# Performance work log

Measured on AMD Instinct MI355X. Metric: run time of the kernel, lower is better.

## Reference

```python
import jax, jax.numpy as jnp
import numpy as np

N = 50000          # nodes
E = 800000         # edges (avg degree 16)
NS = 0.01          # LeakyReLU negative slope
N_CONVS = 3


def setup_inputs() -> dict:
    key = jax.random.key(0)
    ks = jax.random.split(key, 12)
    g = lambda k, s: (jax.random.normal(k, s, dtype=jnp.float32) * 0.05)
    return dict(
        x=jax.random.normal(ks[0], (N, 16), dtype=jnp.float32),
        edge_index=jax.random.randint(ks[1], (2, E), 0, N),
        edge_weight=jax.random.uniform(ks[2], (E, 1), dtype=jnp.float32),
        # prep MLP: Linear(16,64)+LeakyReLU, Linear(64,64)+Tanh
        Wp_in=g(ks[3], (16, 64)), bp_in=jnp.zeros((64,), jnp.float32),
        Wp_h=g(ks[4], (64, 64)), bp_h=jnp.zeros((64,), jnp.float32),
        # per-conv edge projection Linear(edge_dim=1, 64), stacked over 3 convs
        We=g(ks[5], (N_CONVS, 1, 64)), be=jnp.zeros((N_CONVS, 64), jnp.float32),
        # per-conv nn MLP: Linear(64,64)+LeakyReLU, Linear(64,64)+Tanh
        Wm0=g(ks[6], (N_CONVS, 64, 64)), bm0=jnp.zeros((N_CONVS, 64), jnp.float32),
        Wm1=g(ks[7], (N_CONVS, 64, 64)), bm1=jnp.zeros((N_CONVS, 64), jnp.float32),
        # post MLP: Linear(64,64)+LeakyReLU, Linear(64,32)+Tanh
        Wq0=g(ks[8], (64, 64)), bq0=jnp.zeros((64,), jnp.float32),
        Wq1=g(ks[9], (64, 32)), bq1=jnp.zeros((32,), jnp.float32),
    )


def reference(x, edge_index, edge_weight,
              Wp_in, bp_in, Wp_h, bp_h,
              We, be, Wm0, bm0, Wm1, bm1,
              Wq0, bq0, Wq1, bq1):
    lrelu = lambda v: jax.nn.leaky_relu(v, NS)
    # prep MLP (dropout=0 -> no-op)
    h = lrelu(x @ Wp_in + bp_in)
    h = jnp.tanh(h @ Wp_h + bp_h)
    src, dst = edge_index[0], edge_index[1]
    # stacked GINEConv layers (eps=0): out = nn(x + sum_j ReLU(x_j + lin_e(e_ij)))
    for k in range(N_CONVS):
        e = edge_weight @ We[k] + be[k]              # [E,64] edge embedding
        msg = jax.nn.relu(h[src] + e)                # [E,64] gather + fuse
        agg = jax.ops.segment_sum(msg, dst, num_segments=N)  # [N,64] scatter-sum
        z = agg + h                                  # (1+eps)*x with eps=0
        z = lrelu(z @ Wm0[k] + bm0[k])
        h = jnp.tanh(z @ Wm1[k] + bm1[k])
    # post MLP
    z = lrelu(h @ Wq0 + bq0)
    return jnp.tanh(z @ Wq1 + bq1)                   # [N,32]
```

## Files before the change

kernel.cpp:

```cpp
#include <hip/hip_runtime.h>
#include <hip/hip_fp16.h>
#include <math.h>

#define NS 0.01f
#define CAP 48
#define QS (1.f / 65535.f)
#define POISON 0xAAAAAAAAu
#define ZS 72

typedef _Float16 f16;
typedef __attribute__((ext_vector_type(8))) f16 f16x8;
typedef __attribute__((ext_vector_type(4))) float f32x4;

__device__ __forceinline__ float lrelu(float v) { return fmaxf(v, NS * v); }

__device__ __forceinline__ unsigned rel_cnt(unsigned raw) {
    return min(raw, raw - POISON);
}

__global__ void __launch_bounds__(512) build_kernel(
    const int* __restrict__ src, const int* __restrict__ dst,
    const float* __restrict__ ew, int* __restrict__ cnt,
    unsigned* __restrict__ bucket, int E, int fillBlocks,
    const float* __restrict__ x,
    const float* __restrict__ Wp_in, const float* __restrict__ bp_in,
    const float* __restrict__ Wp_h,  const float* __restrict__ bp_h,
    __half* __restrict__ h, int N, int prepBlocks,
    const float* __restrict__ Wm0, const float* __restrict__ Wm1,
    const float* __restrict__ Wq0, const float* __restrict__ Wq1,
    __half* __restrict__ WTh)
{
    __shared__ float zt[64 * 65];
    const int b = (int)blockIdx.x;
    const int t = threadIdx.x;

    if (b < fillBlocks) {
        const int e0 = (b * 512 + t) * 8;
        if (e0 + 7 < E && (E & 7) == 0) {
            const int4   dA = *(const int4*)(dst + e0);
            const int4   dB = *(const int4*)(dst + e0 + 4);
            const int4   sA = *(const int4*)(src + e0);
            const int4   sB = *(const int4*)(src + e0 + 4);
            const float4 wA = *(const float4*)(ew + e0);
            const float4 wB = *(const float4*)(ew + e0 + 4);
            const int   dd[8] = {dA.x, dA.y, dA.z, dA.w, dB.x, dB.y, dB.z, dB.w};
            const int   ss[8] = {sA.x, sA.y, sA.z, sA.w, sB.x, sB.y, sB.z, sB.w};
            const float ww[8] = {wA.x, wA.y, wA.z, wA.w, wB.x, wB.y, wB.z, wB.w};
            unsigned p[8];
            #pragma unroll
            for (int q = 0; q < 8; ++q)
                p[q] = rel_cnt((unsigned)atomicAdd(&cnt[dd[q]], 1));
            #pragma unroll
            for (int q = 0; q < 8; ++q) {
                if (p[q] < CAP) {
                    const unsigned qq = __float2uint_rn(ww[q] * 65535.f) & 0xffffu;
                    __builtin_nontemporal_store(((unsigned)ss[q] << 16) | qq,
                                                &bucket[(size_t)dd[q] * CAP + p[q]]);
                }
            }
        } else {
            for (int e = e0; e < min(e0 + 8, E); ++e) {
                const int d = dst[e];
                const unsigned p = rel_cnt((unsigned)atomicAdd(&cnt[d], 1));
                if (p < CAP) {
                    const unsigned q = __float2uint_rn(ew[e] * 65535.f) & 0xffffu;
                    bucket[(size_t)d * CAP + p] = ((unsigned)src[e] << 16) | q;
                }
            }
        }
        return;
    }
    if (b < fillBlocks + prepBlocks) {
        const int n0 = (b - fillBlocks) * 64;
        #pragma unroll
        for (int r = 0; r < 2; ++r) {
            const int idx = r * 512 + t;
            const int nl = idx >> 4, i = idx & 15;
            const int n = n0 + nl;
            zt[nl * 65 + i] = (n < N) ? x[(size_t)n * 16 + i] : 0.f;
        }
        __syncthreads();
        const int lane = t & 63;
        const int w = __builtin_amdgcn_readfirstlane(t >> 6);
        float zx[16];
        #pragma unroll
        for (int i = 0; i < 16; ++i) zx[i] = zt[lane * 65 + i];
        float y[8];
        #pragma unroll
        for (int jj = 0; jj < 8; ++jj) {
            const int j = w * 8 + jj;
            float a = bp_in[j];
            #pragma unroll
            for (int i = 0; i < 16; ++i) a = fmaf(zx[i], Wp_in[i * 64 + j], a);
            y[jj] = lrelu(a);
        }
        __syncthreads();
        #pragma unroll
        for (int jj = 0; jj < 8; ++jj) zt[lane * 65 + w * 8 + jj] = y[jj];
        __syncthreads();
        #pragma unroll
        for (int jj = 0; jj < 8; ++jj) y[jj] = bp_h[w * 8 + jj];
        #pragma unroll
        for (int half = 0; half < 2; ++half) {
            float zh[32];
            #pragma unroll
            for (int i = 0; i < 32; ++i) zh[i] = zt[lane * 65 + half * 32 + i];
            #pragma unroll
            for (int jj = 0; jj < 8; ++jj) {
                const int j = w * 8 + jj;
                #pragma unroll
                for (int i = 0; i < 32; ++i)
                    y[jj] = fmaf(zh[i], Wp_h[(half * 32 + i) * 64 + j], y[jj]);
            }
        }
        __syncthreads();
        #pragma unroll
        for (int jj = 0; jj < 8; ++jj) zt[lane * 65 + w * 8 + jj] = tanhf(y[jj]);
        __syncthreads();
        #pragma unroll
        for (int r = 0; r < 8; ++r) {
            const int idx = r * 512 + t;
            const int nl = idx >> 6, i = idx & 63;
            const int n = n0 + nl;
            if (n < N) h[(size_t)n * 64 + i] = __float2half(zt[nl * 65 + i]);
        }
        return;
    }
    const int o = (b - fillBlocks - prepBlocks) * 512 + t;
    if (o >= 30720) return;
    float v;
    int d = o;
    if (d < 12288) {
        const int k = d >> 12, r = d & 4095, j = r >> 6, i = r & 63;
        v = Wm0[k * 4096 + i * 64 + j];
    } else if ((d -= 12288) < 12288) {
        const int k = d >> 12, r = d & 4095, j = r >> 6, i = r & 63;
        v = Wm1[k * 4096 + i * 64 + j];
    } else if ((d -= 12288) < 4096) {
        const int j = d >> 6, i = d & 63;
        v = Wq0[i * 64 + j];
    } else {
        d -= 4096;
        const int j = d >> 6, i = d & 63;
        v = Wq1[i * 32 + j];
    }
    WTh[o] = __float2half(v);
}

template<int ACT , int WLO >
__device__ __forceinline__ void mfma_layer64(
    const f16* __restrict__ inH, const f16* __restrict__ inL,
    const __half* __restrict__ WTh, const float* __restrict__ bias,
    int lane, int w, f16* __restrict__ outH, f16* __restrict__ outL)
{
    const int m   = w >> 1;
    const int nb0 = (w & 1) * 2;
    const int ar  = lane & 15;
    const int kg  = lane >> 4;
    const f16* ia = inH + (16 * m + ar) * ZS + kg * 8;
    const f16* il = inL + (16 * m + ar) * ZS + kg * 8;
    const f16x8 aH0 = *(const f16x8*)(ia);
    const f16x8 aH1 = *(const f16x8*)(ia + 32);
    const f16x8 aL0 = *(const f16x8*)(il);
    const f16x8 aL1 = *(const f16x8*)(il + 32);
    #pragma unroll
    for (int tt = 0; tt < 2; ++tt) {
        const int nb = nb0 + tt;
        const f16* wb = (const f16*)WTh + (16 * nb + ar) * 64 + kg * 8;
        const f16x8 b0 = *(const f16x8*)(wb);
        const f16x8 b1 = *(const f16x8*)(wb + 32);
        f32x4 c = {0.f, 0.f, 0.f, 0.f};
        c = __builtin_amdgcn_mfma_f32_16x16x32_f16(aH0, b0, c, 0, 0, 0);
        c = __builtin_amdgcn_mfma_f32_16x16x32_f16(aH1, b1, c, 0, 0, 0);
        c = __builtin_amdgcn_mfma_f32_16x16x32_f16(aL0, b0, c, 0, 0, 0);
        c = __builtin_amdgcn_mfma_f32_16x16x32_f16(aL1, b1, c, 0, 0, 0);
        const float bj = bias[16 * nb + ar];
        #pragma unroll
        for (int r = 0; r < 4; ++r) {
            float y = c[r] + bj;
            y = ACT ? lrelu(y) : tanhf(y);
            const int row = 16 * m + kg * 4 + r;
            const f16 hi = (f16)y;
            outH[row * ZS + 16 * nb + ar] = hi;
            if (WLO) outL[row * ZS + 16 * nb + ar] = (f16)(y - (float)hi);
        }
    }
}

__global__ void __launch_bounds__(512, 8) fused_conv_kernel(
    const __half* __restrict__ hin,
    const int* __restrict__ cnt,
    const unsigned* __restrict__ bucket,
    const float* __restrict__ We_k, const float* __restrict__ be_k,
    const __half* __restrict__ W0Th, const float* __restrict__ b0,
    const __half* __restrict__ W1Th, const float* __restrict__ b1,
    const __half* __restrict__ Wq0Th, const float* __restrict__ bq0,
    const __half* __restrict__ Wq1Th, const float* __restrict__ bq1,
    int do_post, __half* __restrict__ hout, float* __restrict__ out, int N)
{
    __shared__ __align__(16) f16 bAH[64 * ZS];
    __shared__ __align__(16) f16 bAL[64 * ZS];
    __shared__ __align__(16) f16 bBH[64 * ZS];
    __shared__ __align__(16) f16 bBL[64 * ZS];
    const int t = threadIdx.x;
    const int lane = t & 63;
    const int w = __builtin_amdgcn_readfirstlane(t >> 6);
    const int n0 = (int)blockIdx.x * 64;
    const float wej = We_k[lane], bej = be_k[lane];
    const float wqs = wej * QS;

    float acc[8];
    int   len[8];
    const int nb_ = n0 + w * 8;
    #pragma unroll
    for (int s = 0; s < 8; ++s) {
        const int n = nb_ + s;
        if (n < N) {
            acc[s] = __half2float(hin[(size_t)n * 64 + lane]);
            len[s] = __builtin_amdgcn_readfirstlane(
                         (int)min(rel_cnt((unsigned)cnt[n]), (unsigned)CAP));
        } else { acc[s] = 0.f; len[s] = 0; }
    }
    const unsigned* rows = bucket + (size_t)nb_ * CAP;

    int m[4];
    int maxLen = 0;
    #pragma unroll
    for (int pr = 0; pr < 4; ++pr) {
        m[pr] = max(len[2 * pr], len[2 * pr + 1]);
        maxLen = max(maxLen, m[pr]);
    }
    for (int p = 0; p < maxLen; p += 8) {
        #pragma unroll
        for (int pr = 0; pr < 4; ++pr) {
            if (p < m[pr]) {
                const uint4* rA = (const uint4*)(rows + (2 * pr) * CAP);
                const uint4* rB = (const uint4*)(rows + (2 * pr + 1) * CAP);
                const uint4 a0 = rA[p >> 2], a1 = rA[(p >> 2) + 1];
                const uint4 b0_ = rB[p >> 2], b1_ = rB[(p >> 2) + 1];
                unsigned rs[16];
                rs[0] = __builtin_amdgcn_readfirstlane(a0.x);
                rs[1] = __builtin_amdgcn_readfirstlane(a0.y);
                rs[2] = __builtin_amdgcn_readfirstlane(a0.z);
                rs[3] = __builtin_amdgcn_readfirstlane(a0.w);
                rs[4] = __builtin_amdgcn_readfirstlane(a1.x);
                rs[5] = __builtin_amdgcn_readfirstlane(a1.y);
                rs[6] = __builtin_amdgcn_readfirstlane(a1.z);
                rs[7] = __builtin_amdgcn_readfirstlane(a1.w);
                rs[8]  = __builtin_amdgcn_readfirstlane(b0_.x);
                rs[9]  = __builtin_amdgcn_readfirstlane(b0_.y);
                rs[10] = __builtin_amdgcn_readfirstlane(b0_.z);
                rs[11] = __builtin_amdgcn_readfirstlane(b0_.w);
                rs[12] = __builtin_amdgcn_readfirstlane(b1_.x);
                rs[13] = __builtin_amdgcn_readfirstlane(b1_.y);
                rs[14] = __builtin_amdgcn_readfirstlane(b1_.z);
                rs[15] = __builtin_amdgcn_readfirstlane(b1_.w);
                float g[16];
                #pragma unroll
                for (int i = 0; i < 16; ++i)
                    g[i] = __half2float(hin[(size_t)(rs[i] >> 16) * 64 + lane]);
                #pragma unroll
                for (int ss = 0; ss < 2; ++ss) {
                    const int s = 2 * pr + ss;
                    #pragma unroll
                    for (int q = 0; q < 8; ++q) {
                        const float ef = fmaf((float)(rs[ss * 8 + q] & 0xffffu), wqs, bej);
                        const float v  = fmaxf(g[ss * 8 + q] + ef, 0.f);
                        acc[s] += (p + q < len[s]) ? v : 0.f;
                    }
                }
            }
        }
    }
    #pragma unroll
    for (int s = 0; s < 8; ++s) {
        const float a = acc[s];
        const f16 hi = (f16)a;
        bAH[(w * 8 + s) * ZS + lane] = hi;
        bAL[(w * 8 + s) * ZS + lane] = (f16)(a - (float)hi);
    }
    __syncthreads();

    mfma_layer64<1, 1>(bAH, bAL, W0Th, b0, lane, w, bBH, bBL);
    __syncthreads();

    if (!do_post) {
        mfma_layer64<0, 0>(bBH, bBL, W1Th, b1, lane, w, bAH, bAL);
        __syncthreads();
        const int node = t >> 3, ch = t & 7;
        const int n = n0 + node;
        if (n < N)
            *(uint4*)&hout[(size_t)n * 64 + ch * 8] =
                *(const uint4*)&bAH[node * ZS + ch * 8];
        return;
    }
    mfma_layer64<0, 1>(bBH, bBL, W1Th, b1, lane, w, bAH, bAL);
    __syncthreads();
    mfma_layer64<1, 1>(bAH, bAL, Wq0Th, bq0, lane, w, bBH, bBL);
    __syncthreads();
    {
        const int mq  = w >> 1;
        const int nbq = w & 1;
        const int ar  = lane & 15;
        const int kg  = lane >> 4;
        const f16* ia = bBH + (16 * mq + ar) * ZS + kg * 8;
        const f16* il = bBL + (16 * mq + ar) * ZS + kg * 8;
        const f16x8 aH0 = *(const f16x8*)(ia);
        const f16x8 aH1 = *(const f16x8*)(ia + 32);
        const f16x8 aL0 = *(const f16x8*)(il);
        const f16x8 aL1 = *(const f16x8*)(il + 32);
        const f16* wb = (const f16*)Wq1Th + (16 * nbq + ar) * 64 + kg * 8;
        const f16x8 b0_ = *(const f16x8*)(wb);
        const f16x8 b1_ = *(const f16x8*)(wb + 32);
        f32x4 c = {0.f, 0.f, 0.f, 0.f};
        c = __builtin_amdgcn_mfma_f32_16x16x32_f16(aH0, b0_, c, 0, 0, 0);
        c = __builtin_amdgcn_mfma_f32_16x16x32_f16(aH1, b1_, c, 0, 0, 0);
        c = __builtin_amdgcn_mfma_f32_16x16x32_f16(aL0, b0_, c, 0, 0, 0);
        c = __builtin_amdgcn_mfma_f32_16x16x32_f16(aL1, b1_, c, 0, 0, 0);
        const float bj = bq1[16 * nbq + ar];
        #pragma unroll
        for (int r = 0; r < 4; ++r) {
            const float y = tanhf(c[r] + bj);
            const int n = n0 + 16 * mq + kg * 4 + r;
            if (n < N) out[(size_t)n * 32 + 16 * nbq + ar] = y;
        }
    }
}

extern "C" void kernel_launch(void* const* d_in, const int* in_sizes, int n_in,
                              void* d_out, int out_size, void* d_ws, size_t ws_size,
                              hipStream_t stream) {
    const float* x     = (const float*)d_in[0];
    const int*   ei    = (const int*)d_in[1];
    const float* ew    = (const float*)d_in[2];
    const float* Wp_in = (const float*)d_in[3];
    const float* bp_in = (const float*)d_in[4];
    const float* Wp_h  = (const float*)d_in[5];
    const float* bp_h  = (const float*)d_in[6];
    const float* We    = (const float*)d_in[7];
    const float* be    = (const float*)d_in[8];
    const float* Wm0   = (const float*)d_in[9];
    const float* bm0   = (const float*)d_in[10];
    const float* Wm1   = (const float*)d_in[11];
    const float* bm1   = (const float*)d_in[12];
    const float* Wq0   = (const float*)d_in[13];
    const float* bq0   = (const float*)d_in[14];
    const float* Wq1   = (const float*)d_in[15];
    const float* bq1   = (const float*)d_in[16];
    float* out = (float*)d_out;

    const int N = in_sizes[0] / 16;
    const int E = in_sizes[2];
    const int* src = ei;
    const int* dst = ei + E;

    __half*   hA     = (__half*)d_ws;
    __half*   hB     = hA + (size_t)N * 64;
    unsigned* bucket = (unsigned*)(hB + (size_t)N * 64);
    int*      cnt    = (int*)(bucket + (size_t)N * CAP);
    __half*   WTh    = (__half*)(cnt + N);
    __half* Wm0Th = WTh;
    __half* Wm1Th = Wm0Th + 12288;
    __half* Wq0Th = Wm1Th + 12288;
    __half* Wq1Th = Wq0Th + 4096;

    const int fillBlocks = (E + 4095) / 4096;
    const int prepBlocks = (N + 63) / 64;
    const int wtBlocks   = (30720 + 511) / 512;
    const int tileBlocks = (N + 63) / 64;

    build_kernel<<<fillBlocks + prepBlocks + wtBlocks, 512, 0, stream>>>(
        src, dst, ew, cnt, bucket, E, fillBlocks,
        x, Wp_in, bp_in, Wp_h, bp_h, hA, N, prepBlocks,
        Wm0, Wm1, Wq0, Wq1, WTh);

    fused_conv_kernel<<<tileBlocks, 512, 0, stream>>>(
        hA, cnt, bucket, We + 0 * 64, be + 0 * 64,
        Wm0Th + 0 * 4096, bm0 + 0 * 64, Wm1Th + 0 * 4096, bm1 + 0 * 64,
        Wq0Th, bq0, Wq1Th, bq1, 0, hB, out, N);
    fused_conv_kernel<<<tileBlocks, 512, 0, stream>>>(
        hB, cnt, bucket, We + 1 * 64, be + 1 * 64,
        Wm0Th + 1 * 4096, bm0 + 1 * 64, Wm1Th + 1 * 4096, bm1 + 1 * 64,
        Wq0Th, bq0, Wq1Th, bq1, 0, hA, out, N);
    fused_conv_kernel<<<tileBlocks, 512, 0, stream>>>(
        hA, cnt, bucket, We + 2 * 64, be + 2 * 64,
        Wm0Th + 2 * 4096, bm0 + 2 * 64, Wm1Th + 2 * 4096, bm1 + 2 * 64,
        Wq0Th, bq0, Wq1Th, bq1, 1, hB, out, N);
}
```

Measured before the change: 251.5 us.

## Split gather across half-waves with packed half2 loads per lane

Each wave now splits neighbor edges between the two 32-lane halves: each half processes alternate edges and each lane loads a packed half2 (two channels) per neighbor row, instead of all 64 lanes reading one half per lane for every edge. The partial sums are combined with a cross-half shuffle and written as packed pairs into the hi/lo shared buffers. This aims to halve the number of gather load instructions and per-lane conversion work, while making the edge indices per-lane rather than scalar (readfirstlane removed), which may increase VGPR use and address computation.

Measured after the change: 263.1 us. 4.6% more time.

```diff
diff --git a/kernel.cpp b/kernel.cpp
--- a/kernel.cpp
+++ b/kernel.cpp
@@ -206,20 +206,29 @@
     const int lane = t & 63;
     const int w = __builtin_amdgcn_readfirstlane(t >> 6);
     const int n0 = (int)blockIdx.x * 64;
-    const float wej = We_k[lane], bej = be_k[lane];
-    const float wqs = wej * QS;
-
-    float acc[8];
+    const int lh = lane >> 5;
+    const int lf = lane & 31;
+    const unsigned* hin2 = (const unsigned*)hin;
+
+    const float2 wv = *(const float2*)&We_k[2 * lf];
+    const float2 bv = *(const float2*)&be_k[2 * lf];
+    const float wqx = wv.x * QS, wqy = wv.y * QS;
+    const float bex = bv.x, bey = bv.y;
+
+    float accx[8], accy[8];
     int   len[8];
     const int nb_ = n0 + w * 8;
     #pragma unroll
     for (int s = 0; s < 8; ++s) {
         const int n = nb_ + s;
         if (n < N) {
-            acc[s] = __half2float(hin[(size_t)n * 64 + lane]);
-            len[s] = __builtin_amdgcn_readfirstlane(
-                         (int)min(rel_cnt((unsigned)cnt[n]), (unsigned)CAP));
-        } else { acc[s] = 0.f; len[s] = 0; }
+            len[s] = (int)min(rel_cnt((unsigned)cnt[n]), (unsigned)CAP);
+            if (lh == 0) {
+                const __half2 h2 = __builtin_bit_cast(__half2, hin2[(size_t)n * 32 + lf]);
+                accx[s] = __half2float(h2.x);
+                accy[s] = __half2float(h2.y);
+            } else { accx[s] = 0.f; accy[s] = 0.f; }
+        } else { accx[s] = 0.f; accy[s] = 0.f; len[s] = 0; }
     }
     const unsigned* rows = bucket + (size_t)nb_ * CAP;
 
@@ -238,35 +247,32 @@
                 const uint4* rB = (const uint4*)(rows + (2 * pr + 1) * CAP);
                 const uint4 a0 = rA[p >> 2], a1 = rA[(p >> 2) + 1];
                 const uint4 b0_ = rB[p >> 2], b1_ = rB[(p >> 2) + 1];
-                unsigned rs[16];
-                rs[0] = __builtin_amdgcn_readfirstlane(a0.x);
-                rs[1] = __builtin_amdgcn_readfirstlane(a0.y);
-                rs[2] = __builtin_amdgcn_readfirstlane(a0.z);
-                rs[3] = __builtin_amdgcn_readfirstlane(a0.w);
-                rs[4] = __builtin_amdgcn_readfirstlane(a1.x);
-                rs[5] = __builtin_amdgcn_readfirstlane(a1.y);
-                rs[6] = __builtin_amdgcn_readfirstlane(a1.z);
-                rs[7] = __builtin_amdgcn_readfirstlane(a1.w);
-                rs[8]  = __builtin_amdgcn_readfirstlane(b0_.x);
-                rs[9]  = __builtin_amdgcn_readfirstlane(b0_.y);
-                rs[10] = __builtin_amdgcn_readfirstlane(b0_.z);
-                rs[11] = __builtin_amdgcn_readfirstlane(b0_.w);
-                rs[12] = __builtin_amdgcn_readfirstlane(b1_.x);
-                rs[13] = __builtin_amdgcn_readfirstlane(b1_.y);
-                rs[14] = __builtin_amdgcn_readfirstlane(b1_.z);
-                rs[15] = __builtin_amdgcn_readfirstlane(b1_.w);
-                float g[16];
+                unsigned se[8];
+                se[0] = lh ? a0.y : a0.x;
+                se[1] = lh ? a0.w : a0.z;
+                se[2] = lh ? a1.y : a1.x;
+                se[3] = lh ? a1.w : a1.z;
+                se[4] = lh ? b0_.y : b0_.x;
+                se[5] = lh ? b0_.w : b0_.z;
+                se[6] = lh ? b1_.y : b1_.x;
+                se[7] = lh ? b1_.w : b1_.z;
+                unsigned g[8];
                 #pragma unroll
-                for (int i = 0; i < 16; ++i)
-                    g[i] = __half2float(hin[(size_t)(rs[i] >> 16) * 64 + lane]);
+                for (int i = 0; i < 8; ++i)
+                    g[i] = hin2[(size_t)(se[i] >> 16) * 32 + lf];
                 #pragma unroll
                 for (int ss = 0; ss < 2; ++ss) {
                     const int s = 2 * pr + ss;
                     #pragma unroll
-                    for (int q = 0; q < 8; ++q) {
-                        const float ef = fmaf((float)(rs[ss * 8 + q] & 0xffffu), wqs, bej);
-                        const float v  = fmaxf(g[ss * 8 + q] + ef, 0.f);
-                        acc[s] += (p + q < len[s]) ? v : 0.f;
+                    for (int i = 0; i < 4; ++i) {
+                        const unsigned r = se[ss * 4 + i];
+                        const __half2 h2 = __builtin_bit_cast(__half2, g[ss * 4 + i]);
+                        const float q16 = (float)(r & 0xffffu);
+                        const float vx = fmaxf(__half2float(h2.x) + fmaf(q16, wqx, bex), 0.f);
+                        const float vy = fmaxf(__half2float(h2.y) + fmaf(q16, wqy, bey), 0.f);
+                        const bool ok = (p + 2 * i + lh) < len[s];
+                        accx[s] += ok ? vx : 0.f;
+                        accy[s] += ok ? vy : 0.f;
                     }
                 }
             }
@@ -274,10 +280,24 @@
     }
     #pragma unroll
     for (int s = 0; s < 8; ++s) {
-        const float a = acc[s];
-        const f16 hi = (f16)a;
-        bAH[(w * 8 + s) * ZS + lane] = hi;
-        bAL[(w * 8 + s) * ZS + lane] = (f16)(a - (float)hi);
+        accx[s] += __shfl_xor(accx[s], 32);
+        accy[s] += __shfl_xor(accy[s], 32);
+    }
+    {
+        const int sB = lh * 4;
+        #pragma unroll
+        for (int i = 0; i < 4; ++i) {
+            const int s = sB + i;
+            const float ax = accx[s], ay = accy[s];
+            const f16 hx = (f16)ax, hy = (f16)ay;
+            const f16 lx = (f16)(ax - (float)hx), ly = (f16)(ay - (float)hy);
+            const unsigned hp = ((unsigned)__builtin_bit_cast(unsigned short, hy) << 16)
+                               | (unsigned)__builtin_bit_cast(unsigned short, hx);
+            const unsigned lp = ((unsigned)__builtin_bit_cast(unsigned short, ly) << 16)
+                               | (unsigned)__builtin_bit_cast(unsigned short, lx);
+            *(unsigned*)&bAH[(w * 8 + s) * ZS + 2 * lf] = hp;
+            *(unsigned*)&bAL[(w * 8 + s) * ZS + 2 * lf] = lp;
+        }
     }
     __syncthreads();
 
```
